# Kernel tuning notes

Hardware: AMD Instinct MI355X
Metric: run time of the kernel (lower is better)

Reference implementation:

```python
import jax, jax.numpy as jnp
import numpy as np
import math

DM, DP, P = 1024, 128, 256
B, S = 8, 4096

def setup_inputs() -> dict:
    key = jax.random.key(0)
    ks = jax.random.split(key, 7)
    sd = lambda fan_in: 1.0 / math.sqrt(fan_in)
    return {
        "x": jax.random.normal(ks[0], (B, S, DM), jnp.float32),
        "prim_embeds": jax.random.normal(ks[1], (P, DP), jnp.float32),
        "Wq": jax.random.normal(ks[2], (DP, DM), jnp.float32) * sd(DM),
        "Wk": jax.random.normal(ks[3], (DP, DP), jnp.float32) * sd(DP),
        "Wv": jax.random.normal(ks[4], (DP, DP), jnp.float32) * sd(DP),
        "Wo": jax.random.normal(ks[5], (DM, DP), jnp.float32) * sd(DP),
        "gate_w": jax.random.normal(ks[6], (1, DM), jnp.float32) * sd(DM),
        "gate_b": jnp.zeros((1,), jnp.float32),
    }

def reference(x, prim_embeds, Wq, Wk, Wv, Wo, gate_w, gate_b):
    # q: [B,S,dp]; k,v: [P,dp]
    q = jnp.einsum('bsm,pm->bsp', x, Wq)          # p here = d_prim
    k = prim_embeds @ Wk.T                         # [P, dp]
    v = prim_embeds @ Wv.T                         # [P, dp]
    scale = 1.0 / math.sqrt(q.shape[-1])
    scores = jnp.einsum('bsd,pd->bsp', q, k) * scale  # [B,S,P]
    attn = jax.nn.softmax(scores, axis=-1)
    ctx = jnp.einsum('bsp,pd->bsd', attn, v)       # [B,S,dp]
    out = jnp.einsum('bsd,md->bsm', ctx, Wo)       # [B,S,dm]
    gate = jax.nn.sigmoid(jnp.einsum('bsm,om->bso', x, gate_w) + gate_b)  # [B,S,1]
    return gate * out
```

## Files before the change

kernel.cpp:

```cpp
#include <hip/hip_runtime.h>
#include <hip/hip_bf16.h>

typedef unsigned short ushort_t;
typedef __attribute__((ext_vector_type(8))) short short8;
typedef __attribute__((ext_vector_type(8))) unsigned short ushort8;
typedef __attribute__((ext_vector_type(4))) float f32x4;

#define MFMA16(a,b,c) __builtin_amdgcn_mfma_f32_16x16x32_bf16((a),(b),(c),0,0,0)

__device__ __forceinline__ ushort_t f2bf(float f) {
  unsigned int u = __builtin_bit_cast(unsigned int, f);
  u += 0x7FFFu + ((u >> 16) & 1u);
  return (ushort_t)(u >> 16);
}
__device__ __forceinline__ unsigned int pack2bf(float a, float b) {
  unsigned int ua = __builtin_bit_cast(unsigned int, a);
  unsigned int ub = __builtin_bit_cast(unsigned int, b);
  ua += 0x7FFFu + ((ua >> 16) & 1u);
  ub += 0x7FFFu + ((ub >> 16) & 1u);
  return (ua >> 16) | (ub & 0xFFFF0000u);
}

#define DMd 1024
#define DPd 128
#define PPd 256

#define KWQ_OFF 0
#define KWQ_SIZE (8*17*4*512)
#define VWO_OFF KWQ_SIZE
#define VWO_SIZE (64*8*512)
#define KV_BYTE_OFF ((size_t)(KWQ_SIZE + VWO_SIZE) * 2)

__global__ void prep1_kernel(const float* __restrict__ prim, const float* __restrict__ Wk,
                             const float* __restrict__ Wv, ushort_t* __restrict__ ws) {
  float* kf = (float*)((char*)ws + KV_BYTE_OFF);
  float* vf = kf + 32768;
  int idx = blockIdx.x * 256 + threadIdx.x;
  int mat = idx >> 15, rem = idx & 32767;
  int p = rem >> 7, d = rem & 127;
  const float4* pr = (const float4*)(prim + p * 128);
  const float4* wr = (const float4*)((mat ? Wv : Wk) + d * 128);
  float s0 = 0.f, s1 = 0.f;
  #pragma unroll
  for (int j = 0; j < 32; j += 2) {
    float4 a = pr[j], b = wr[j];
    s0 += a.x*b.x + a.y*b.y + a.z*b.z + a.w*b.w;
    float4 a2 = pr[j+1], b2 = wr[j+1];
    s1 += a2.x*b2.x + a2.y*b2.y + a2.z*b2.z + a2.w*b2.w;
  }
  (mat ? vf : kf)[rem] = s0 + s1;
}

__global__ void prep2_kernel(const float* __restrict__ Wq, const float* __restrict__ Wo,
                             const float* __restrict__ gate_w, ushort_t* __restrict__ ws) {
  const float* kf = (const float*)((const char*)ws + KV_BYTE_OFF);
  const float* vf = kf + 32768;
  const int b = blockIdx.x, t = threadIdx.x;
  if (b < 68) {
    const int p  = (b >> 2) * 16 + (t >> 4);
    const int m0 = (b & 3) * 256 + (t & 15) * 16;
    float acc[16];
    #pragma unroll
    for (int j = 0; j < 16; ++j) acc[j] = 0.f;
    if (p < 256) {
      const float* kp = kf + p * 128;
      for (int d = 0; d < 128; ++d) {
        float kv = kp[d];
        const float4* wr = (const float4*)(Wq + (size_t)d * 1024 + m0);
        #pragma unroll
        for (int q = 0; q < 4; ++q) {
          float4 w = wr[q];
          acc[q*4+0] += kv * w.x; acc[q*4+1] += kv * w.y;
          acc[q*4+2] += kv * w.z; acc[q*4+3] += kv * w.w;
        }
      }
    } else if (p == 256) {
      #pragma unroll
      for (int j = 0; j < 16; ++j) acc[j] = gate_w[m0 + j];
    }
    const int ct = p >> 4, l16p = p & 15;
    const int c = m0 >> 7, k4 = (m0 >> 5) & 3, q0 = (m0 >> 3) & 3;
    ushort8 u0, u1;
    #pragma unroll
    for (int j = 0; j < 8; ++j) { u0[j] = f2bf(acc[j]); u1[j] = f2bf(acc[8+j]); }
    size_t base = ((size_t)(c * 17 + ct) * 4 + k4) * 512;
    *(ushort8*)&ws[KWQ_OFF + base + (size_t)(q0 * 16 + l16p) * 8]       = u0;
    *(ushort8*)&ws[KWQ_OFF + base + (size_t)((q0 + 1) * 16 + l16p) * 8] = u1;
  } else {
    __shared__ float vs[16 * 128];
    const int bb = b - 68;
    const int p0 = (bb >> 2) * 16;
    const int m  = (bb & 3) * 256 + t;
    {
      int row = t >> 4, col = (t & 15) * 8;
      const float4* src = (const float4*)(vf + (p0 + row) * 128 + col);
      float4 a0 = src[0], a1 = src[1];
      *(float4*)&vs[row * 128 + col]     = a0;
      *(float4*)&vs[row * 128 + col + 4] = a1;
    }
    __syncthreads();
    float acc[16];
    #pragma unroll
    for (int j = 0; j < 16; ++j) acc[j] = 0.f;
    const float4* wr = (const float4*)(Wo + (size_t)m * 128);
    for (int d4 = 0; d4 < 32; ++d4) {
      float4 w = wr[d4];
      #pragma unroll
      for (int pp = 0; pp < 16; ++pp) {
        float4 v4 = *(const float4*)&vs[pp * 128 + d4 * 4];
        acc[pp] += w.x*v4.x + w.y*v4.y + w.z*v4.z + w.w*v4.w;
      }
    }
    const int ctg = m >> 4, l16m = m & 15;
    ushort8 u0, u1;
    #pragma unroll
    for (int j = 0; j < 8; ++j) { u0[j] = f2bf(acc[j]); u1[j] = f2bf(acc[8+j]); }
    const int pA = p0, pB = p0 + 8;
    *(ushort8*)&ws[VWO_OFF + ((size_t)(ctg*8 + (pA>>5))*512) + (size_t)(((pA>>3)&3)*16 + l16m)*8] = u0;
    *(ushort8*)&ws[VWO_OFF + ((size_t)(ctg*8 + (pB>>5))*512) + (size_t)(((pB>>3)&3)*16 + l16m)*8] = u1;
  }
}

#define LDX 136
#define LDSLAB 264

__global__ __launch_bounds__(256, 2) void fused_kernel(
    const float* __restrict__ x, const float* __restrict__ gate_b,
    const ushort_t* __restrict__ ws, float* __restrict__ out)
{
  __shared__ __align__(16) char smem[64 * LDSLAB * 2 + 64 * 4 * 4 * 2 + 64 * 4];
  ushort_t* xt       = (ushort_t*)smem;
  ushort_t* slab     = (ushort_t*)smem;
  float*    pmax     = (float*)(smem + 64 * LDSLAB * 2);
  float*    psum     = pmax + 256;
  float*    gate_lds = psum + 256;

  const int t = threadIdx.x, wid = t >> 6, lane = t & 63;
  const int quad = lane >> 4, l16 = lane & 15;
  const int tok0 = blockIdx.x * 64;

  f32x4 acc[4][5];
  #pragma unroll
  for (int rt = 0; rt < 4; ++rt)
    #pragma unroll
    for (int ctl = 0; ctl < 5; ++ctl) acc[rt][ctl] = (f32x4){0.f,0.f,0.f,0.f};

  for (int c = 0; c < 8; ++c) {
    if (c) __syncthreads();
    #pragma unroll
    for (int i = 0; i < 8; ++i) {
      int flat = i * 1024 + t * 4;
      int row = flat >> 7, col = flat & 127;
      float4 f = *(const float4*)(x + (size_t)(tok0 + row) * 1024 + c * 128 + col);
      unsigned int pk0 = pack2bf(f.x, f.y), pk1 = pack2bf(f.z, f.w);
      unsigned long long dv = (unsigned long long)pk0 | ((unsigned long long)pk1 << 32);
      *(unsigned long long*)&xt[row * LDX + col] = dv;
    }
    __syncthreads();
    #pragma unroll
    for (int k4 = 0; k4 < 4; ++k4) {
      short8 a[4];
      #pragma unroll
      for (int rt = 0; rt < 4; ++rt)
        a[rt] = *(const short8*)&xt[(rt * 16 + l16) * LDX + k4 * 32 + quad * 8];
      #pragma unroll
      for (int ctl = 0; ctl < 5; ++ctl) {
        if (ctl == 4 && wid != 3) continue;
        const int ct = wid * 4 + ctl;
        short8 bfr = *(const short8*)&ws[KWQ_OFF +
            ((size_t)(c * 17 + ct) * 4 + k4) * 512 + (size_t)lane * 8];
        #pragma unroll
        for (int rt = 0; rt < 4; ++rt) acc[rt][ctl] = MFMA16(a[rt], bfr, acc[rt][ctl]);
      }
    }
  }

  const float SC = 0.08838834764831845f * 1.44269504088896f;
  float Mx[4][4];
  #pragma unroll
  for (int rt = 0; rt < 4; ++rt)
    #pragma unroll
    for (int r = 0; r < 4; ++r) {
      float m = acc[rt][0][r];
      #pragma unroll
      for (int ctl = 1; ctl < 4; ++ctl) m = fmaxf(m, acc[rt][ctl][r]);
      #pragma unroll
      for (int msk = 1; msk < 16; msk <<= 1) m = fmaxf(m, __shfl_xor(m, msk, 64));
      Mx[rt][r] = m;
    }
  if (l16 == 0) {
    #pragma unroll
    for (int rt = 0; rt < 4; ++rt)
      #pragma unroll
      for (int r = 0; r < 4; ++r)
        pmax[(rt * 16 + quad * 4 + r) * 4 + wid] = Mx[rt][r];
  }
  __syncthreads();
  float Mf[4][4];
  #pragma unroll
  for (int rt = 0; rt < 4; ++rt)
    #pragma unroll
    for (int r = 0; r < 4; ++r) {
      f32x4 pm = *(f32x4*)&pmax[(rt * 16 + quad * 4 + r) * 4];
      Mf[rt][r] = fmaxf(fmaxf(pm[0], pm[1]), fmaxf(pm[2], pm[3]));
    }
  float Sm[4][4];
  #pragma unroll
  for (int rt = 0; rt < 4; ++rt)
    #pragma unroll
    for (int r = 0; r < 4; ++r) Sm[rt][r] = 0.f;
  #pragma unroll
  for (int rt = 0; rt < 4; ++rt)
    #pragma unroll
    for (int ctl = 0; ctl < 4; ++ctl)
      #pragma unroll
      for (int r = 0; r < 4; ++r) {
        float e = exp2f((acc[rt][ctl][r] - Mf[rt][r]) * SC);
        acc[rt][ctl][r] = e;
        Sm[rt][r] += e;
      }
  #pragma unroll
  for (int rt = 0; rt < 4; ++rt)
    #pragma unroll
    for (int r = 0; r < 4; ++r) {
      #pragma unroll
      for (int msk = 1; msk < 16; msk <<= 1) Sm[rt][r] += __shfl_xor(Sm[rt][r], msk, 64);
    }
  if (l16 == 0) {
    #pragma unroll
    for (int rt = 0; rt < 4; ++rt)
      #pragma unroll
      for (int r = 0; r < 4; ++r)
        psum[(rt * 16 + quad * 4 + r) * 4 + wid] = Sm[rt][r];
    if (wid == 3) {
      float gb = gate_b[0];
      #pragma unroll
      for (int rt = 0; rt < 4; ++rt)
        #pragma unroll
        for (int r = 0; r < 4; ++r) {
          float lg = acc[rt][4][r] + gb;
          gate_lds[rt * 16 + quad * 4 + r] = 1.f / (1.f + __expf(-lg));
        }
    }
  }
  __syncthreads();
  float inv[4][4];
  #pragma unroll
  for (int rt = 0; rt < 4; ++rt)
    #pragma unroll
    for (int r = 0; r < 4; ++r) {
      f32x4 ps = *(f32x4*)&psum[(rt * 16 + quad * 4 + r) * 4];
      inv[rt][r] = 1.f / (ps[0] + ps[1] + ps[2] + ps[3]);
    }

  #pragma unroll
  for (int rt = 0; rt < 4; ++rt)
    #pragma unroll
    for (int ctl = 0; ctl < 4; ++ctl)
      #pragma unroll
      for (int r = 0; r < 4; ++r)
        slab[(rt * 16 + quad * 4 + r) * LDSLAB + (wid * 4 + ctl) * 16 + l16] =
            f2bf(acc[rt][ctl][r] * inv[rt][r]);
  __syncthreads();

  short8 af[4][8];
  #pragma unroll
  for (int rt = 0; rt < 4; ++rt)
    #pragma unroll
    for (int k8 = 0; k8 < 8; ++k8)
      af[rt][k8] = *(const short8*)&slab[(rt * 16 + l16) * LDSLAB + k8 * 32 + quad * 8];
  float g[4][4];
  #pragma unroll
  for (int rt = 0; rt < 4; ++rt)
    #pragma unroll
    for (int r = 0; r < 4; ++r) g[rt][r] = gate_lds[rt * 16 + quad * 4 + r];

  const int n0 = wid * 256;
  for (int nt = 0; nt < 16; ++nt) {
    const int ctg = (n0 >> 4) + nt;
    short8 bf[8];
    #pragma unroll
    for (int k8 = 0; k8 < 8; ++k8)
      bf[k8] = *(const short8*)&ws[VWO_OFF + ((size_t)(ctg * 8 + k8) * 512) + (size_t)lane * 8];
    f32x4 oa[4];
    #pragma unroll
    for (int rt = 0; rt < 4; ++rt) oa[rt] = (f32x4){0.f,0.f,0.f,0.f};
    #pragma unroll
    for (int rt = 0; rt < 4; ++rt)
      #pragma unroll
      for (int k8 = 0; k8 < 8; ++k8)
        oa[rt] = MFMA16(af[rt][k8], bf[k8], oa[rt]);
    #pragma unroll
    for (int rt = 0; rt < 4; ++rt)
      #pragma unroll
      for (int r = 0; r < 4; ++r)
        out[(size_t)(tok0 + rt * 16 + quad * 4 + r) * 1024 + n0 + nt * 16 + l16] =
            oa[rt][r] * g[rt][r];
  }
}

extern "C" void kernel_launch(void* const* d_in, const int* in_sizes, int n_in,
                              void* d_out, int out_size, void* d_ws, size_t ws_size,
                              hipStream_t stream) {
  const float* x    = (const float*)d_in[0];
  const float* prim = (const float*)d_in[1];
  const float* Wq   = (const float*)d_in[2];
  const float* Wk   = (const float*)d_in[3];
  const float* Wv   = (const float*)d_in[4];
  const float* Wo   = (const float*)d_in[5];
  const float* gw   = (const float*)d_in[6];
  const float* gb   = (const float*)d_in[7];
  float* out = (float*)d_out;
  ushort_t* ws = (ushort_t*)d_ws;

  prep1_kernel<<<256, 256, 0, stream>>>(prim, Wk, Wv, ws);
  prep2_kernel<<<132, 256, 0, stream>>>(Wq, Wo, gw, ws);
  fused_kernel<<<512, 256, 0, stream>>>(x, gb, ws, out);
}
```

Measured before the change: 355.7 us.

## Halve token tile, double-buffer x loads, fold gate into softmax scale

New measurement: 328.0 us. -7.8%, faster.

```diff
diff --git a/kernel.cpp b/kernel.cpp
--- a/kernel.cpp
+++ b/kernel.cpp
@@ -124,45 +124,57 @@
 #define LDX 136
 #define LDSLAB 264
 
-__global__ __launch_bounds__(256, 2) void fused_kernel(
+__global__ __launch_bounds__(256, 4) void fused_kernel(
     const float* __restrict__ x, const float* __restrict__ gate_b,
     const ushort_t* __restrict__ ws, float* __restrict__ out)
 {
-  __shared__ __align__(16) char smem[64 * LDSLAB * 2 + 64 * 4 * 4 * 2 + 64 * 4];
-  ushort_t* xt       = (ushort_t*)smem;
+  __shared__ __align__(16) char smem[2 * 32 * LDX * 2 + 32 * 4 * 4 * 2 + 32 * 4];
+  ushort_t* xt0      = (ushort_t*)smem;
+  ushort_t* xt1      = xt0 + 32 * LDX;
   ushort_t* slab     = (ushort_t*)smem;
-  float*    pmax     = (float*)(smem + 64 * LDSLAB * 2);
-  float*    psum     = pmax + 256;
-  float*    gate_lds = psum + 256;
+  float*    pmax     = (float*)(smem + 2 * 32 * LDX * 2);
+  float*    psum     = pmax + 128;
+  float*    gate_lds = psum + 128;
 
   const int t = threadIdx.x, wid = t >> 6, lane = t & 63;
   const int quad = lane >> 4, l16 = lane & 15;
-  const int tok0 = blockIdx.x * 64;
-
-  f32x4 acc[4][5];
-  #pragma unroll
-  for (int rt = 0; rt < 4; ++rt)
+  const int tok0 = blockIdx.x * 32;
+
+  f32x4 acc[2][5];
+  #pragma unroll
+  for (int rt = 0; rt < 2; ++rt)
     #pragma unroll
     for (int ctl = 0; ctl < 5; ++ctl) acc[rt][ctl] = (f32x4){0.f,0.f,0.f,0.f};
 
+  #pragma unroll
+  for (int i = 0; i < 4; ++i) {
+    int flat = i * 1024 + t * 4;
+    int row = flat >> 7, col = flat & 127;
+    float4 fv = *(const float4*)(x + (size_t)(tok0 + row) * 1024 + col);
+    unsigned int pk0 = pack2bf(fv.x, fv.y), pk1 = pack2bf(fv.z, fv.w);
+    *(unsigned long long*)&xt0[row * LDX + col] =
+        (unsigned long long)pk0 | ((unsigned long long)pk1 << 32);
+  }
+  __syncthreads();
+
   for (int c = 0; c < 8; ++c) {
-    if (c) __syncthreads();
-    #pragma unroll
-    for (int i = 0; i < 8; ++i) {
-      int flat = i * 1024 + t * 4;
-      int row = flat >> 7, col = flat & 127;
-      float4 f = *(const float4*)(x + (size_t)(tok0 + row) * 1024 + c * 128 + col);
-      unsigned int pk0 = pack2bf(f.x, f.y), pk1 = pack2bf(f.z, f.w);
-      unsigned long long dv = (unsigned long long)pk0 | ((unsigned long long)pk1 << 32);
-      *(unsigned long long*)&xt[row * LDX + col] = dv;
-    }
-    __syncthreads();
+    ushort_t* cur = (c & 1) ? xt1 : xt0;
+    ushort_t* nxt = (c & 1) ? xt0 : xt1;
+    float4 fv[4];
+    if (c < 7) {
+      #pragma unroll
+      for (int i = 0; i < 4; ++i) {
+        int flat = i * 1024 + t * 4;
+        int row = flat >> 7, col = flat & 127;
+        fv[i] = *(const float4*)(x + (size_t)(tok0 + row) * 1024 + (c + 1) * 128 + col);
+      }
+    }
     #pragma unroll
     for (int k4 = 0; k4 < 4; ++k4) {
-      short8 a[4];
-      #pragma unroll
-      for (int rt = 0; rt < 4; ++rt)
-        a[rt] = *(const short8*)&xt[(rt * 16 + l16) * LDX + k4 * 32 + quad * 8];
+      short8 a[2];
+      #pragma unroll
+      for (int rt = 0; rt < 2; ++rt)
+        a[rt] = *(const short8*)&cur[(rt * 16 + l16) * LDX + k4 * 32 + quad * 8];
       #pragma unroll
       for (int ctl = 0; ctl < 5; ++ctl) {
         if (ctl == 4 && wid != 3) continue;
@@ -170,15 +182,26 @@
         short8 bfr = *(const short8*)&ws[KWQ_OFF +
             ((size_t)(c * 17 + ct) * 4 + k4) * 512 + (size_t)lane * 8];
         #pragma unroll
-        for (int rt = 0; rt < 4; ++rt) acc[rt][ctl] = MFMA16(a[rt], bfr, acc[rt][ctl]);
-      }
+        for (int rt = 0; rt < 2; ++rt) acc[rt][ctl] = MFMA16(a[rt], bfr, acc[rt][ctl]);
+      }
+    }
+    if (c < 7) {
+      #pragma unroll
+      for (int i = 0; i < 4; ++i) {
+        int flat = i * 1024 + t * 4;
+        int row = flat >> 7, col = flat & 127;
+        unsigned int pk0 = pack2bf(fv[i].x, fv[i].y), pk1 = pack2bf(fv[i].z, fv[i].w);
+        *(unsigned long long*)&nxt[row * LDX + col] =
+            (unsigned long long)pk0 | ((unsigned long long)pk1 << 32);
+      }
+      __syncthreads();
     }
   }
 
   const float SC = 0.08838834764831845f * 1.44269504088896f;
-  float Mx[4][4];
-  #pragma unroll
-  for (int rt = 0; rt < 4; ++rt)
+  float Mx[2][4];
+  #pragma unroll
+  for (int rt = 0; rt < 2; ++rt)
     #pragma unroll
     for (int r = 0; r < 4; ++r) {
       float m = acc[rt][0][r];
@@ -190,27 +213,27 @@
     }
   if (l16 == 0) {
     #pragma unroll
-    for (int rt = 0; rt < 4; ++rt)
+    for (int rt = 0; rt < 2; ++rt)
       #pragma unroll
       for (int r = 0; r < 4; ++r)
         pmax[(rt * 16 + quad * 4 + r) * 4 + wid] = Mx[rt][r];
   }
   __syncthreads();
-  float Mf[4][4];
-  #pragma unroll
-  for (int rt = 0; rt < 4; ++rt)
+  float Mf[2][4];
+  #pragma unroll
+  for (int rt = 0; rt < 2; ++rt)
     #pragma unroll
     for (int r = 0; r < 4; ++r) {
       f32x4 pm = *(f32x4*)&pmax[(rt * 16 + quad * 4 + r) * 4];
       Mf[rt][r] = fmaxf(fmaxf(pm[0], pm[1]), fmaxf(pm[2], pm[3]));
     }
-  float Sm[4][4];
-  #pragma unroll
-  for (int rt = 0; rt < 4; ++rt)
+  float Sm[2][4];
+  #pragma unroll
+  for (int rt = 0; rt < 2; ++rt)
     #pragma unroll
     for (int r = 0; r < 4; ++r) Sm[rt][r] = 0.f;
   #pragma unroll
-  for (int rt = 0; rt < 4; ++rt)
+  for (int rt = 0; rt < 2; ++rt)
     #pragma unroll
     for (int ctl = 0; ctl < 4; ++ctl)
       #pragma unroll
@@ -220,7 +243,7 @@
         Sm[rt][r] += e;
       }
   #pragma unroll
-  for (int rt = 0; rt < 4; ++rt)
+  for (int rt = 0; rt < 2; ++rt)
     #pragma unroll
     for (int r = 0; r < 4; ++r) {
       #pragma unroll
@@ -228,14 +251,14 @@
     }
   if (l16 == 0) {
     #pragma unroll
-    for (int rt = 0; rt < 4; ++rt)
+    for (int rt = 0; rt < 2; ++rt)
       #pragma unroll
       for (int r = 0; r < 4; ++r)
         psum[(rt * 16 + quad * 4 + r) * 4 + wid] = Sm[rt][r];
     if (wid == 3) {
       float gb = gate_b[0];
       #pragma unroll
-      for (int rt = 0; rt < 4; ++rt)
+      for (int rt = 0; rt < 2; ++rt)
         #pragma unroll
         for (int r = 0; r < 4; ++r) {
           float lg = acc[rt][4][r] + gb;
@@ -244,36 +267,32 @@
     }
   }
   __syncthreads();
-  float inv[4][4];
-  #pragma unroll
-  for (int rt = 0; rt < 4; ++rt)
+  float scl[2][4];
+  #pragma unroll
+  for (int rt = 0; rt < 2; ++rt)
     #pragma unroll
     for (int r = 0; r < 4; ++r) {
       f32x4 ps = *(f32x4*)&psum[(rt * 16 + quad * 4 + r) * 4];
-      inv[rt][r] = 1.f / (ps[0] + ps[1] + ps[2] + ps[3]);
-    }
-
-  #pragma unroll
-  for (int rt = 0; rt < 4; ++rt)
+      float g = gate_lds[rt * 16 + quad * 4 + r];
+      scl[rt][r] = g / (ps[0] + ps[1] + ps[2] + ps[3]);
+    }
+
+  #pragma unroll
+  for (int rt = 0; rt < 2; ++rt)
     #pragma unroll
     for (int ctl = 0; ctl < 4; ++ctl)
       #pragma unroll
       for (int r = 0; r < 4; ++r)
         slab[(rt * 16 + quad * 4 + r) * LDSLAB + (wid * 4 + ctl) * 16 + l16] =
-            f2bf(acc[rt][ctl][r] * inv[rt][r]);
+            f2bf(acc[rt][ctl][r] * scl[rt][r]);
   __syncthreads();
 
-  short8 af[4][8];
-  #pragma unroll
-  for (int rt = 0; rt < 4; ++rt)
+  short8 af[2][8];
+  #pragma unroll
+  for (int rt = 0; rt < 2; ++rt)
     #pragma unroll
     for (int k8 = 0; k8 < 8; ++k8)
       af[rt][k8] = *(const short8*)&slab[(rt * 16 + l16) * LDSLAB + k8 * 32 + quad * 8];
-  float g[4][4];
-  #pragma unroll
-  for (int rt = 0; rt < 4; ++rt)
-    #pragma unroll
-    for (int r = 0; r < 4; ++r) g[rt][r] = gate_lds[rt * 16 + quad * 4 + r];
 
   const int n0 = wid * 256;
   for (int nt = 0; nt < 16; ++nt) {
@@ -282,20 +301,20 @@
     #pragma unroll
     for (int k8 = 0; k8 < 8; ++k8)
       bf[k8] = *(const short8*)&ws[VWO_OFF + ((size_t)(ctg * 8 + k8) * 512) + (size_t)lane * 8];
-    f32x4 oa[4];
-    #pragma unroll
-    for (int rt = 0; rt < 4; ++rt) oa[rt] = (f32x4){0.f,0.f,0.f,0.f};
-    #pragma unroll
-    for (int rt = 0; rt < 4; ++rt)
+    f32x4 oa[2];
+    #pragma unroll
+    for (int rt = 0; rt < 2; ++rt) oa[rt] = (f32x4){0.f,0.f,0.f,0.f};
+    #pragma unroll
+    for (int rt = 0; rt < 2; ++rt)
       #pragma unroll
       for (int k8 = 0; k8 < 8; ++k8)
         oa[rt] = MFMA16(af[rt][k8], bf[k8], oa[rt]);
     #pragma unroll
-    for (int rt = 0; rt < 4; ++rt)
+    for (int rt = 0; rt < 2; ++rt)
       #pragma unroll
       for (int r = 0; r < 4; ++r)
-        out[(size_t)(tok0 + rt * 16 + quad * 4 + r) * 1024 + n0 + nt * 16 + l16] =
-            oa[rt][r] * g[rt][r];
+        __builtin_nontemporal_store(oa[rt][r],
+            &out[(size_t)(tok0 + rt * 16 + quad * 4 + r) * 1024 + n0 + nt * 16 + l16]);
   }
 }
 
@@ -315,5 +334,5 @@
 
   prep1_kernel<<<256, 256, 0, stream>>>(prim, Wk, Wv, ws);
   prep2_kernel<<<132, 256, 0, stream>>>(Wq, Wo, gw, ws);
-  fused_kernel<<<512, 256, 0, stream>>>(x, gb, ws, out);
-}
+  fused_kernel<<<1024, 256, 0, stream>>>(x, gb, ws, out);
+}
```
